# Kernel tuning notes

Measured on AMD Instinct MI355X. Metric: run time of the kernel, lower is better.

Reference implementation:

```python
import jax, jax.numpy as jnp
import numpy as np

N_NODES = 100000
N_EDGES = 1600000
IN_F = 64
HIDDEN = [64, 64, 32]


def _glorot(key, shape):
    limit = float(np.sqrt(6.0 / (shape[0] + shape[1])))
    return jax.random.uniform(key, shape, jnp.float32, -limit, limit)


def setup_inputs() -> dict:
    key = jax.random.key(0)
    ks = jax.random.split(key, 5)
    x = jax.random.normal(ks[0], (N_NODES, IN_F), jnp.float32)
    edge_index = jax.random.randint(ks[1], (2, N_EDGES), 0, N_NODES, jnp.int64)
    dims = [IN_F] + HIDDEN
    params = {}
    for i in range(len(HIDDEN)):
        params[f"W{i+1}"] = _glorot(ks[2 + i], (dims[i], dims[i + 1]))
        params[f"b{i+1}"] = jnp.zeros((dims[i + 1],), jnp.float32)
    return {"x": x, "edge_index": edge_index, **params}


def _gcn_layer(x, src, dst, norm, W, b, n):
    # PyG GCNConv: linear transform, then normalized scatter-sum aggregation, then bias
    h = x @ W                                  # [N, out]
    msg = norm[:, None] * h[src]               # gather + edge scaling, [E+N, out]
    out = jax.ops.segment_sum(msg, dst, num_segments=n)
    return out + b


def reference(x, edge_index, W1, b1, W2, b2, W3, b3):
    n = x.shape[0]
    # add self-loops (GCNConv default add_self_loops=True)
    loops = jnp.arange(n, dtype=edge_index.dtype)
    src = jnp.concatenate([edge_index[0], loops])
    dst = jnp.concatenate([edge_index[1], loops])
    # symmetric normalization: deg over destination (col), norm = d^-1/2[src]*d^-1/2[dst]
    deg = jax.ops.segment_sum(jnp.ones_like(src, x.dtype), dst, num_segments=n)
    dinv = jnp.where(deg > 0, jax.lax.rsqrt(deg), 0.0)
    norm = dinv[src] * dinv[dst]
    h = jax.nn.relu(_gcn_layer(x, src, dst, norm, W1, b1, n))
    h = jax.nn.relu(_gcn_layer(h, src, dst, norm, W2, b2, n))
    return _gcn_layer(h, src, dst, norm, W3, b3, n)
```

## Files before the change

### kernel.cpp

```cpp
#include <hip/hip_runtime.h>
#include <hip/hip_bf16.h>


#define BLOCK 256
#define NBUCKET 512
#define CHUNK 4096
#define SLOT 4608
#define MAX_NPB 256

typedef float f32x4 __attribute__((ext_vector_type(4)));

__device__ __forceinline__ float4 fma4(float s, float4 a, float4 b) {
  return make_float4(fmaf(s, a.x, b.x), fmaf(s, a.y, b.y),
                     fmaf(s, a.z, b.z), fmaf(s, a.w, b.w));
}

__device__ __forceinline__ unsigned int bf16r(float f) {
  unsigned int u = __float_as_uint(f);
  u += 0x7fffu + ((u >> 16) & 1u);
  return u >> 16;
}

__device__ __forceinline__ void acc_bf8(float4& lo, float4& hi, uint4 u) {
  lo.x += __uint_as_float(u.x << 16);
  lo.y += __uint_as_float(u.x & 0xffff0000u);
  lo.z += __uint_as_float(u.y << 16);
  lo.w += __uint_as_float(u.y & 0xffff0000u);
  hi.x += __uint_as_float(u.z << 16);
  hi.y += __uint_as_float(u.z & 0xffff0000u);
  hi.z += __uint_as_float(u.w << 16);
  hi.w += __uint_as_float(u.w & 0xffff0000u);
}


__global__ __launch_bounds__(BLOCK) void binning_kernel(
    const int* __restrict__ src, const int* __restrict__ dst,
    int* __restrict__ bcursor, int* __restrict__ binned, int e, int npb) {
  __shared__ int h[NBUCKET];
  __shared__ int base[NBUCKET];
  for (int i = threadIdx.x; i < NBUCKET; i += BLOCK) h[i] = 0;
  __syncthreads();
  const int cbase = blockIdx.x * CHUNK;
#pragma unroll
  for (int k = 0; k < CHUNK; k += BLOCK * 4) {
    int i = cbase + k + threadIdx.x * 4;
    if (i + 3 < e) {
      int4 d4 = *(const int4*)(dst + i);
      atomicAdd(&h[d4.x / npb], 1);
      atomicAdd(&h[d4.y / npb], 1);
      atomicAdd(&h[d4.z / npb], 1);
      atomicAdd(&h[d4.w / npb], 1);
    } else {
      for (int t = 0; t < 4; ++t)
        if (i + t < e) atomicAdd(&h[dst[i + t] / npb], 1);
    }
  }
  __syncthreads();
  for (int i = threadIdx.x; i < NBUCKET; i += BLOCK) {
    int c = h[i];
    base[i] = c ? atomicAdd(&bcursor[i], c) : 0;
    h[i] = 0;
  }
  __syncthreads();
#pragma unroll
  for (int k = 0; k < CHUNK; k += BLOCK * 4) {
    int i = cbase + k + threadIdx.x * 4;
    if (i + 3 < e) {
      int4 d4 = *(const int4*)(dst + i);
      int4 s4 = *(const int4*)(src + i);
      int b0 = d4.x / npb, b1 = d4.y / npb, b2 = d4.z / npb, b3 = d4.w / npb;
      int o0 = atomicAdd(&h[b0], 1);
      int o1 = atomicAdd(&h[b1], 1);
      int o2 = atomicAdd(&h[b2], 1);
      int o3 = atomicAdd(&h[b3], 1);
      binned[b0 * SLOT + base[b0] + o0] = s4.x | ((d4.x - b0 * npb) << 17);
      binned[b1 * SLOT + base[b1] + o1] = s4.y | ((d4.y - b1 * npb) << 17);
      binned[b2 * SLOT + base[b2] + o2] = s4.z | ((d4.z - b2 * npb) << 17);
      binned[b3 * SLOT + base[b3] + o3] = s4.w | ((d4.w - b3 * npb) << 17);
    } else {
      for (int t = 0; t < 4; ++t) {
        if (i + t < e) {
          int d = dst[i + t];
          int bkt = d / npb;
          int lofs = atomicAdd(&h[bkt], 1);
          binned[bkt * SLOT + base[bkt] + lofs] =
              src[i + t] | ((d - bkt * npb) << 17);
        }
      }
    }
  }
}

__global__ __launch_bounds__(BLOCK) void bucket_build(
    const int* __restrict__ binned, const int* __restrict__ bcursor,
    int* __restrict__ offs, int* __restrict__ cnt, float* __restrict__ dinv,
    int* __restrict__ csr_src, int n, int npb) {
  __shared__ int nhist[MAX_NPB];
  __shared__ int noff[MAX_NPB];
  __shared__ int lcsr[SLOT];
  const int b = blockIdx.x;
  const int node_base = b * npb;
  const int nodes = min(npb, n - node_base);
  if (nodes <= 0) return;
  const int ebase = b * SLOT;
  const int ecnt = bcursor[b];
  for (int i = threadIdx.x; i < npb; i += BLOCK) nhist[i] = 0;
  __syncthreads();
  for (int i = threadIdx.x; i < ecnt; i += BLOCK)
    atomicAdd(&nhist[binned[ebase + i] >> 17], 1);
  __syncthreads();
  if (threadIdx.x < 64) {
    const int lane = threadIdx.x;
    const int bi = lane * 4;
    int v0 = (bi + 0 < nodes) ? nhist[bi + 0] : 0;
    int v1 = (bi + 1 < nodes) ? nhist[bi + 1] : 0;
    int v2 = (bi + 2 < nodes) ? nhist[bi + 2] : 0;
    int v3 = (bi + 3 < nodes) ? nhist[bi + 3] : 0;
    int tsum = v0 + v1 + v2 + v3;
    int s = tsum;
#pragma unroll
    for (int o = 1; o < 64; o <<= 1) {
      int u = __shfl_up(s, o, 64);
      if (lane >= o) s += u;
    }
    int texcl = s - tsum;
    if (bi + 0 < nodes) noff[bi + 0] = texcl;
    if (bi + 1 < nodes) noff[bi + 1] = texcl + v0;
    if (bi + 2 < nodes) noff[bi + 2] = texcl + v0 + v1;
    if (bi + 3 < nodes) noff[bi + 3] = texcl + v0 + v1 + v2;
  }
  __syncthreads();
  for (int i = threadIdx.x; i < nodes; i += BLOCK) {
    int c = nhist[i];
    offs[node_base + i] = ebase + noff[i];
    cnt[node_base + i] = c;
    dinv[node_base + i] = rsqrtf((float)(c + 1));
  }
  __syncthreads();
  for (int i = threadIdx.x; i < ecnt; i += BLOCK) {
    int v = binned[ebase + i];
    int pos = atomicAdd(&noff[v >> 17], 1);
    lcsr[pos] = v & 0x1ffff;
  }
  __syncthreads();
  for (int i = threadIdx.x; i < ecnt; i += BLOCK)
    csr_src[ebase + i] = lcsr[i];
}


__global__ __launch_bounds__(BLOCK) void gemm1_kernel(
    const float* __restrict__ x, const float* __restrict__ W,
    const float* __restrict__ dinv, unsigned short* __restrict__ hbf, int n) {
  __shared__ float Ws[64 * 64];
  for (int i = threadIdx.x * 4; i < 64 * 64; i += BLOCK * 4)
    *(float4*)(Ws + i) = *(const float4*)(W + i);
  __syncthreads();
  const int row = blockIdx.x * 16 + (int)(threadIdx.x >> 4);
  const int c4 = (threadIdx.x & 15) * 4;
  if (row >= n) return;
  const float* xr = x + (size_t)row * 64;
  float4 acc = make_float4(0.f, 0.f, 0.f, 0.f);
#pragma unroll
  for (int k = 0; k < 64; k += 4) {
    f32x4 xn = __builtin_nontemporal_load((const f32x4*)(xr + k));
    float4 w0 = *(const float4*)(Ws + (k + 0) * 64 + c4);
    float4 w1 = *(const float4*)(Ws + (k + 1) * 64 + c4);
    float4 w2 = *(const float4*)(Ws + (k + 2) * 64 + c4);
    float4 w3 = *(const float4*)(Ws + (k + 3) * 64 + c4);
    acc = fma4(xn.x, w0, acc);
    acc = fma4(xn.y, w1, acc);
    acc = fma4(xn.z, w2, acc);
    acc = fma4(xn.w, w3, acc);
  }
  float d = dinv[row];
  uint2 packed;
  packed.x = bf16r(d * acc.x) | (bf16r(d * acc.y) << 16);
  packed.y = bf16r(d * acc.z) | (bf16r(d * acc.w) << 16);
  *(uint2*)(hbf + (size_t)row * 64 + c4) = packed;
}

__global__ __launch_bounds__(BLOCK) void fused_agg_gemm64(
    const unsigned short* __restrict__ hin, const int* __restrict__ csr_src,
    const int* __restrict__ offs, const int* __restrict__ cnt,
    const float* __restrict__ dinv, const float* __restrict__ bias,
    const float* __restrict__ Wn, unsigned short* __restrict__ hout, int n) {
  __shared__ float Ws[64 * 64];
  __shared__ float vrow[16][68];
  for (int i = threadIdx.x * 4; i < 64 * 64; i += BLOCK * 4)
    *(float4*)(Ws + i) = *(const float4*)(Wn + i);
  __syncthreads();
  const int g = threadIdx.x >> 4;
  const int lane16 = threadIdx.x & 15;
  const int colgrp = lane16 & 7;
  const int half = lane16 >> 3;
  const int c8 = colgrp * 8;
  const int node = blockIdx.x * 16 + g;
  const bool valid = node < n;
  float dnode = 0.f;
  if (valid) {
    const int start = offs[node];
    const int cn = cnt[node];
    const unsigned short* hcol = hin + c8;
    float4 l0 = make_float4(0.f, 0.f, 0.f, 0.f), h0 = l0;
    float4 l1 = l0, h1 = l0, l2 = l0, h2 = l0, l3 = l0, h3 = l0;
    if (half == 0)
      acc_bf8(l0, h0, *(const uint4*)(hcol + (size_t)node * 64));
    int j = half * 4;
    for (; j + 4 <= cn; j += 8) {
      int s0 = csr_src[start + j + 0];
      int s1 = csr_src[start + j + 1];
      int s2 = csr_src[start + j + 2];
      int s3 = csr_src[start + j + 3];
      uint4 u0 = *(const uint4*)(hcol + (size_t)s0 * 64);
      uint4 u1 = *(const uint4*)(hcol + (size_t)s1 * 64);
      uint4 u2 = *(const uint4*)(hcol + (size_t)s2 * 64);
      uint4 u3 = *(const uint4*)(hcol + (size_t)s3 * 64);
      acc_bf8(l0, h0, u0);
      acc_bf8(l1, h1, u1);
      acc_bf8(l2, h2, u2);
      acc_bf8(l3, h3, u3);
    }
    if (j < cn) {
      int rem = cn - j;
      int s0 = csr_src[start + j];
      acc_bf8(l1, h1, *(const uint4*)(hcol + (size_t)s0 * 64));
      if (rem > 1) {
        int s1 = csr_src[start + j + 1];
        acc_bf8(l2, h2, *(const uint4*)(hcol + (size_t)s1 * 64));
      }
      if (rem > 2) {
        int s2 = csr_src[start + j + 2];
        acc_bf8(l3, h3, *(const uint4*)(hcol + (size_t)s2 * 64));
      }
    }
    float4 alo = make_float4((l0.x + l1.x) + (l2.x + l3.x),
                             (l0.y + l1.y) + (l2.y + l3.y),
                             (l0.z + l1.z) + (l2.z + l3.z),
                             (l0.w + l1.w) + (l2.w + l3.w));
    float4 ahi = make_float4((h0.x + h1.x) + (h2.x + h3.x),
                             (h0.y + h1.y) + (h2.y + h3.y),
                             (h0.z + h1.z) + (h2.z + h3.z),
                             (h0.w + h1.w) + (h2.w + h3.w));
    alo.x += __shfl_xor(alo.x, 8); alo.y += __shfl_xor(alo.y, 8);
    alo.z += __shfl_xor(alo.z, 8); alo.w += __shfl_xor(alo.w, 8);
    ahi.x += __shfl_xor(ahi.x, 8); ahi.y += __shfl_xor(ahi.y, 8);
    ahi.z += __shfl_xor(ahi.z, 8); ahi.w += __shfl_xor(ahi.w, 8);
    dnode = dinv[node];
    if (half == 0) {
      float4 blo = *(const float4*)(bias + c8);
      float4 bhi = *(const float4*)(bias + c8 + 4);
      float4 vlo = make_float4(fmaxf(fmaf(dnode, alo.x, blo.x), 0.f),
                               fmaxf(fmaf(dnode, alo.y, blo.y), 0.f),
                               fmaxf(fmaf(dnode, alo.z, blo.z), 0.f),
                               fmaxf(fmaf(dnode, alo.w, blo.w), 0.f));
      float4 vhi = make_float4(fmaxf(fmaf(dnode, ahi.x, bhi.x), 0.f),
                               fmaxf(fmaf(dnode, ahi.y, bhi.y), 0.f),
                               fmaxf(fmaf(dnode, ahi.z, bhi.z), 0.f),
                               fmaxf(fmaf(dnode, ahi.w, bhi.w), 0.f));
      *(float4*)(&vrow[g][c8]) = vlo;
      *(float4*)(&vrow[g][c8 + 4]) = vhi;
    }
  }
  if (valid) {
    const int cc = lane16 * 4;
    float4 a0 = make_float4(0.f, 0.f, 0.f, 0.f);
#pragma unroll
    for (int k = 0; k < 64; k += 4) {
      float4 rv = *(const float4*)(&vrow[g][k]);
      a0 = fma4(rv.x, *(const float4*)(Ws + (k + 0) * 64 + cc), a0);
      a0 = fma4(rv.y, *(const float4*)(Ws + (k + 1) * 64 + cc), a0);
      a0 = fma4(rv.z, *(const float4*)(Ws + (k + 2) * 64 + cc), a0);
      a0 = fma4(rv.w, *(const float4*)(Ws + (k + 3) * 64 + cc), a0);
    }
    uint2 packed;
    packed.x = bf16r(dnode * a0.x) | (bf16r(dnode * a0.y) << 16);
    packed.y = bf16r(dnode * a0.z) | (bf16r(dnode * a0.w) << 16);
    *(uint2*)(hout + (size_t)node * 64 + cc) = packed;
  }
}

__global__ __launch_bounds__(BLOCK) void fused_agg_gemm32(
    const unsigned short* __restrict__ hin, const int* __restrict__ csr_src,
    const int* __restrict__ offs, const int* __restrict__ cnt,
    const float* __restrict__ dinv, const float* __restrict__ bias,
    const float* __restrict__ Wn, unsigned short* __restrict__ hout, int n) {
  __shared__ float Ws[64 * 32];
  __shared__ float vrow[32][68];
  for (int i = threadIdx.x * 4; i < 64 * 32; i += BLOCK * 4)
    *(float4*)(Ws + i) = *(const float4*)(Wn + i);
  __syncthreads();
  const int g = threadIdx.x >> 3;
  const int lane8 = threadIdx.x & 7;
  const int c8 = lane8 * 8;
  const int node = blockIdx.x * 32 + g;
  const bool valid = node < n;
  float dnode = 0.f;
  if (valid) {
    const int start = offs[node];
    const int cn = cnt[node];
    const unsigned short* hcol = hin + c8;
    float4 l0 = make_float4(0.f, 0.f, 0.f, 0.f), h0 = l0;
    float4 l1 = l0, h1 = l0, l2 = l0, h2 = l0, l3 = l0, h3 = l0;
    acc_bf8(l0, h0, *(const uint4*)(hcol + (size_t)node * 64));
    int j = 0;
    for (; j + 4 <= cn; j += 4) {
      int s0 = csr_src[start + j + 0];
      int s1 = csr_src[start + j + 1];
      int s2 = csr_src[start + j + 2];
      int s3 = csr_src[start + j + 3];
      uint4 u0 = *(const uint4*)(hcol + (size_t)s0 * 64);
      uint4 u1 = *(const uint4*)(hcol + (size_t)s1 * 64);
      uint4 u2 = *(const uint4*)(hcol + (size_t)s2 * 64);
      uint4 u3 = *(const uint4*)(hcol + (size_t)s3 * 64);
      acc_bf8(l0, h0, u0);
      acc_bf8(l1, h1, u1);
      acc_bf8(l2, h2, u2);
      acc_bf8(l3, h3, u3);
    }
    if (j + 2 <= cn) {
      int s0 = csr_src[start + j + 0];
      int s1 = csr_src[start + j + 1];
      uint4 u0 = *(const uint4*)(hcol + (size_t)s0 * 64);
      uint4 u1 = *(const uint4*)(hcol + (size_t)s1 * 64);
      acc_bf8(l1, h1, u0);
      acc_bf8(l2, h2, u1);
      j += 2;
    }
    if (j < cn) {
      int s0 = csr_src[start + j];
      acc_bf8(l3, h3, *(const uint4*)(hcol + (size_t)s0 * 64));
    }
    float4 alo = make_float4((l0.x + l1.x) + (l2.x + l3.x),
                             (l0.y + l1.y) + (l2.y + l3.y),
                             (l0.z + l1.z) + (l2.z + l3.z),
                             (l0.w + l1.w) + (l2.w + l3.w));
    float4 ahi = make_float4((h0.x + h1.x) + (h2.x + h3.x),
                             (h0.y + h1.y) + (h2.y + h3.y),
                             (h0.z + h1.z) + (h2.z + h3.z),
                             (h0.w + h1.w) + (h2.w + h3.w));
    dnode = dinv[node];
    float4 blo = *(const float4*)(bias + c8);
    float4 bhi = *(const float4*)(bias + c8 + 4);
    float4 vlo = make_float4(fmaxf(fmaf(dnode, alo.x, blo.x), 0.f),
                             fmaxf(fmaf(dnode, alo.y, blo.y), 0.f),
                             fmaxf(fmaf(dnode, alo.z, blo.z), 0.f),
                             fmaxf(fmaf(dnode, alo.w, blo.w), 0.f));
    float4 vhi = make_float4(fmaxf(fmaf(dnode, ahi.x, bhi.x), 0.f),
                             fmaxf(fmaf(dnode, ahi.y, bhi.y), 0.f),
                             fmaxf(fmaf(dnode, ahi.z, bhi.z), 0.f),
                             fmaxf(fmaf(dnode, ahi.w, bhi.w), 0.f));
    *(float4*)(&vrow[g][c8]) = vlo;
    *(float4*)(&vrow[g][c8 + 4]) = vhi;
  }
  if (valid) {
    const int cc = lane8 * 4;
    float4 a0 = make_float4(0.f, 0.f, 0.f, 0.f);
#pragma unroll
    for (int k = 0; k < 64; k += 4) {
      float4 rv = *(const float4*)(&vrow[g][k]);
      a0 = fma4(rv.x, *(const float4*)(Ws + (k + 0) * 32 + cc), a0);
      a0 = fma4(rv.y, *(const float4*)(Ws + (k + 1) * 32 + cc), a0);
      a0 = fma4(rv.z, *(const float4*)(Ws + (k + 2) * 32 + cc), a0);
      a0 = fma4(rv.w, *(const float4*)(Ws + (k + 3) * 32 + cc), a0);
    }
    uint2 packed;
    packed.x = bf16r(dnode * a0.x) | (bf16r(dnode * a0.y) << 16);
    packed.y = bf16r(dnode * a0.z) | (bf16r(dnode * a0.w) << 16);
    *(uint2*)(hout + (size_t)node * 32 + cc) = packed;
  }
}

__global__ __launch_bounds__(BLOCK) void agg3_kernel(
    const unsigned short* __restrict__ hbf, const int* __restrict__ csr_src,
    const int* __restrict__ offs, const int* __restrict__ cnt,
    const float* __restrict__ dinv, const float* __restrict__ bias,
    float* __restrict__ out, int n) {
  constexpr int F = 32;
  const int node = blockIdx.x * 64 + (int)(threadIdx.x >> 2);
  const int c8 = (threadIdx.x & 3) * 8;
  if (node >= n) return;
  const int start = offs[node];
  const int cn = cnt[node];
  const unsigned short* hcol = hbf + c8;
  float4 l0 = make_float4(0.f, 0.f, 0.f, 0.f), h0 = l0;
  float4 l1 = l0, h1 = l0, l2 = l0, h2 = l0, l3 = l0, h3 = l0;
  acc_bf8(l0, h0, *(const uint4*)(hcol + (size_t)node * F));
  int j = 0;
  for (; j + 4 <= cn; j += 4) {
    int s0 = csr_src[start + j + 0];
    int s1 = csr_src[start + j + 1];
    int s2 = csr_src[start + j + 2];
    int s3 = csr_src[start + j + 3];
    uint4 u0 = *(const uint4*)(hcol + (size_t)s0 * F);
    uint4 u1 = *(const uint4*)(hcol + (size_t)s1 * F);
    uint4 u2 = *(const uint4*)(hcol + (size_t)s2 * F);
    uint4 u3 = *(const uint4*)(hcol + (size_t)s3 * F);
    acc_bf8(l0, h0, u0);
    acc_bf8(l1, h1, u1);
    acc_bf8(l2, h2, u2);
    acc_bf8(l3, h3, u3);
  }
  if (j + 2 <= cn) {
    int s0 = csr_src[start + j + 0];
    int s1 = csr_src[start + j + 1];
    uint4 u0 = *(const uint4*)(hcol + (size_t)s0 * F);
    uint4 u1 = *(const uint4*)(hcol + (size_t)s1 * F);
    acc_bf8(l1, h1, u0);
    acc_bf8(l2, h2, u1);
    j += 2;
  }
  if (j < cn) {
    int s0 = csr_src[start + j];
    acc_bf8(l3, h3, *(const uint4*)(hcol + (size_t)s0 * F));
  }
  float4 alo = make_float4((l0.x + l1.x) + (l2.x + l3.x),
                           (l0.y + l1.y) + (l2.y + l3.y),
                           (l0.z + l1.z) + (l2.z + l3.z),
                           (l0.w + l1.w) + (l2.w + l3.w));
  float4 ahi = make_float4((h0.x + h1.x) + (h2.x + h3.x),
                           (h0.y + h1.y) + (h2.y + h3.y),
                           (h0.z + h1.z) + (h2.z + h3.z),
                           (h0.w + h1.w) + (h2.w + h3.w));
  float d = dinv[node];
  float4 blo = *(const float4*)(bias + c8);
  float4 bhi = *(const float4*)(bias + c8 + 4);
  f32x4 vlo = {fmaf(d, alo.x, blo.x), fmaf(d, alo.y, blo.y),
               fmaf(d, alo.z, blo.z), fmaf(d, alo.w, blo.w)};
  f32x4 vhi = {fmaf(d, ahi.x, bhi.x), fmaf(d, ahi.y, bhi.y),
               fmaf(d, ahi.z, bhi.z), fmaf(d, ahi.w, bhi.w)};
  float* op = out + (size_t)node * F + c8;
  __builtin_nontemporal_store(vlo, (f32x4*)op);
  __builtin_nontemporal_store(vhi, (f32x4*)(op + 4));
}

static inline size_t align_up(size_t v, size_t a) { return (v + a - 1) & ~(a - 1); }

extern "C" void kernel_launch(void* const* d_in, const int* in_sizes, int n_in,
                              void* d_out, int out_size, void* d_ws, size_t ws_size,
                              hipStream_t stream) {
  const float* x = (const float*)d_in[0];
  const int* edge_index = (const int*)d_in[1];
  const float* W1 = (const float*)d_in[2];
  const float* b1 = (const float*)d_in[3];
  const float* W2 = (const float*)d_in[4];
  const float* b2 = (const float*)d_in[5];
  const float* W3 = (const float*)d_in[6];
  const float* b3 = (const float*)d_in[7];
  float* out = (float*)d_out;

  const int n = in_sizes[0] / 64;
  const int e = in_sizes[1] / 2;
  const int* e_src = edge_index;
  const int* e_dst = edge_index + e;
  const int npb = (n + NBUCKET - 1) / NBUCKET;

  char* ws = (char*)d_ws;
  size_t off = 0;
  int* bcursor = (int*)(ws + off); off = align_up(off + NBUCKET * 4, 512);
  int* offs    = (int*)(ws + off); off = align_up(off + (size_t)n * 4, 512);
  int* cnt     = (int*)(ws + off); off = align_up(off + (size_t)n * 4, 512);
  float* dinv  = (float*)(ws + off); off = align_up(off + (size_t)n * 4, 512);
  int* binned  = (int*)(ws + off); off = align_up(off + (size_t)NBUCKET * SLOT * 4, 512);
  int* csr_src = (int*)(ws + off); off = align_up(off + (size_t)NBUCKET * SLOT * 4, 512);
  unsigned short* hbuf_a = (unsigned short*)(ws + off);
  off = align_up(off + (size_t)n * 64 * 2, 512);
  unsigned short* hbuf_b = (unsigned short*)(ws + off);
  off = align_up(off + (size_t)n * 64 * 2, 512);
  (void)ws_size;

  const int gC = (e + CHUNK - 1) / CHUNK;

  hipMemsetAsync(bcursor, 0, NBUCKET * 4, stream);
  binning_kernel<<<gC, BLOCK, 0, stream>>>(e_src, e_dst, bcursor, binned, e, npb);
  bucket_build<<<NBUCKET, BLOCK, 0, stream>>>(binned, bcursor, offs, cnt, dinv,
                                              csr_src, n, npb);

  gemm1_kernel<<<(n + 15) / 16, BLOCK, 0, stream>>>(x, W1, dinv, hbuf_a, n);
  fused_agg_gemm64<<<(n + 15) / 16, BLOCK, 0, stream>>>(
      hbuf_a, csr_src, offs, cnt, dinv, b1, W2, hbuf_b, n);
  fused_agg_gemm32<<<(n + 31) / 32, BLOCK, 0, stream>>>(
      hbuf_b, csr_src, offs, cnt, dinv, b2, W3, hbuf_a, n);
  agg3_kernel<<<(n + 63) / 64, BLOCK, 0, stream>>>(hbuf_a, csr_src, offs, cnt,
                                                   dinv, b3, out, n);
}
```

Before: 249.0 us.

## Use split-bf16 MFMA for dense transforms in all three GCN layers

Replaces the scalar FP32 FMA GEMMs in gemm1 and the two fused aggregate+GEMM kernels with MFMA 16x16x32 bf16 instructions. Both operands are split into hi/lo bf16 parts, and three MFMAs per K-chunk keep accuracy close to FP32. A small prep kernel pre-transposes and splits the weights once per call, which removes the per-block FP32 weight staging in LDS. The cost is extra split arithmetic, an added launch, and output stores that become scattered 2-byte writes instead of packed 8-byte ones.

```diff
diff --git a/kernel.cpp b/kernel.cpp
--- a/kernel.cpp
+++ b/kernel.cpp
@@ -9,6 +9,7 @@
 #define MAX_NPB 256
 
 typedef float f32x4 __attribute__((ext_vector_type(4)));
+typedef short bf16x8 __attribute__((ext_vector_type(8)));
 
 __device__ __forceinline__ float4 fma4(float s, float4 a, float4 b) {
   return make_float4(fmaf(s, a.x, b.x), fmaf(s, a.y, b.y),
@@ -19,6 +20,13 @@
   unsigned int u = __float_as_uint(f);
   u += 0x7fffu + ((u >> 16) & 1u);
   return u >> 16;
+}
+
+__device__ __forceinline__ void bsplit(float v, unsigned int& h,
+                                       unsigned int& l) {
+  h = bf16r(v);
+  float r = v - __uint_as_float(h << 16);
+  l = bf16r(r);
 }
 
 __device__ __forceinline__ void acc_bf8(float4& lo, float4& hi, uint4 u) {
@@ -147,48 +155,101 @@
     csr_src[ebase + i] = lcsr[i];
 }
 
+__global__ __launch_bounds__(BLOCK) void wprep_kernel(
+    const float* __restrict__ W1, const float* __restrict__ W2,
+    const float* __restrict__ W3, unsigned short* __restrict__ Wt) {
+  int t = blockIdx.x * BLOCK + threadIdx.x;
+  float v;
+  int hi_off, lo_off;
+  if (t < 4096) {
+    int nn = t >> 6, k = t & 63;
+    v = W1[k * 64 + nn];
+    hi_off = t;
+    lo_off = 4096 + t;
+  } else if (t < 8192) {
+    int i = t - 4096;
+    int nn = i >> 6, k = i & 63;
+    v = W2[k * 64 + nn];
+    hi_off = 8192 + i;
+    lo_off = 12288 + i;
+  } else {
+    int i = t - 8192;
+    if (i >= 2048) return;
+    int nn = i >> 6, k = i & 63;
+    v = W3[k * 32 + nn];
+    hi_off = 16384 + i;
+    lo_off = 18432 + i;
+  }
+  unsigned int h, l;
+  bsplit(v, h, l);
+  Wt[hi_off] = (unsigned short)h;
+  Wt[lo_off] = (unsigned short)l;
+}
+
 
 __global__ __launch_bounds__(BLOCK) void gemm1_kernel(
-    const float* __restrict__ x, const float* __restrict__ W,
+    const float* __restrict__ x, const unsigned short* __restrict__ Wt,
     const float* __restrict__ dinv, unsigned short* __restrict__ hbf, int n) {
-  __shared__ float Ws[64 * 64];
-  for (int i = threadIdx.x * 4; i < 64 * 64; i += BLOCK * 4)
-    *(float4*)(Ws + i) = *(const float4*)(W + i);
-  __syncthreads();
-  const int row = blockIdx.x * 16 + (int)(threadIdx.x >> 4);
+  __shared__ unsigned short Ahi[16][72];
+  __shared__ unsigned short Alo[16][72];
+  __shared__ float dvs[16];
+  const int r16 = threadIdx.x >> 4;
   const int c4 = (threadIdx.x & 15) * 4;
-  if (row >= n) return;
-  const float* xr = x + (size_t)row * 64;
-  float4 acc = make_float4(0.f, 0.f, 0.f, 0.f);
+  const int node = blockIdx.x * 16 + r16;
+  const int wv = threadIdx.x >> 6;
+  const int fr = threadIdx.x & 15;
+  const int fq = (threadIdx.x >> 4) & 3;
+  const unsigned short* wb = Wt + ((wv * 16 + fr) * 64) + fq * 8;
+  bf16x8 bh0 = *(const bf16x8*)(wb);
+  bf16x8 bh1 = *(const bf16x8*)(wb + 32);
+  bf16x8 bl0 = *(const bf16x8*)(wb + 4096);
+  bf16x8 bl1 = *(const bf16x8*)(wb + 4096 + 32);
+  uint2 ph = make_uint2(0u, 0u), pl = make_uint2(0u, 0u);
+  if (node < n) {
+    f32x4 xv =
+        __builtin_nontemporal_load((const f32x4*)(x + (size_t)node * 64 + c4));
+    unsigned int h0, l0, h1, l1, h2, l2, h3, l3;
+    bsplit(xv.x, h0, l0);
+    bsplit(xv.y, h1, l1);
+    bsplit(xv.z, h2, l2);
+    bsplit(xv.w, h3, l3);
+    ph = make_uint2(h0 | (h1 << 16), h2 | (h3 << 16));
+    pl = make_uint2(l0 | (l1 << 16), l2 | (l3 << 16));
+  }
+  *(uint2*)(&Ahi[r16][c4]) = ph;
+  *(uint2*)(&Alo[r16][c4]) = pl;
+  if ((threadIdx.x & 15) == 0) dvs[r16] = (node < n) ? dinv[node] : 0.f;
+  __syncthreads();
+  bf16x8 ah0 = *(const bf16x8*)(&Ahi[fr][fq * 8]);
+  bf16x8 ah1 = *(const bf16x8*)(&Ahi[fr][fq * 8 + 32]);
+  bf16x8 aL0 = *(const bf16x8*)(&Alo[fr][fq * 8]);
+  bf16x8 aL1 = *(const bf16x8*)(&Alo[fr][fq * 8 + 32]);
+  f32x4 acc = {0.f, 0.f, 0.f, 0.f};
+  acc = __builtin_amdgcn_mfma_f32_16x16x32_bf16(ah0, bh0, acc, 0, 0, 0);
+  acc = __builtin_amdgcn_mfma_f32_16x16x32_bf16(aL0, bh0, acc, 0, 0, 0);
+  acc = __builtin_amdgcn_mfma_f32_16x16x32_bf16(ah0, bl0, acc, 0, 0, 0);
+  acc = __builtin_amdgcn_mfma_f32_16x16x32_bf16(ah1, bh1, acc, 0, 0, 0);
+  acc = __builtin_amdgcn_mfma_f32_16x16x32_bf16(aL1, bh1, acc, 0, 0, 0);
+  acc = __builtin_amdgcn_mfma_f32_16x16x32_bf16(ah1, bl1, acc, 0, 0, 0);
+  const int col = wv * 16 + fr;
 #pragma unroll
-  for (int k = 0; k < 64; k += 4) {
-    f32x4 xn = __builtin_nontemporal_load((const f32x4*)(xr + k));
-    float4 w0 = *(const float4*)(Ws + (k + 0) * 64 + c4);
-    float4 w1 = *(const float4*)(Ws + (k + 1) * 64 + c4);
-    float4 w2 = *(const float4*)(Ws + (k + 2) * 64 + c4);
-    float4 w3 = *(const float4*)(Ws + (k + 3) * 64 + c4);
-    acc = fma4(xn.x, w0, acc);
-    acc = fma4(xn.y, w1, acc);
-    acc = fma4(xn.z, w2, acc);
-    acc = fma4(xn.w, w3, acc);
-  }
-  float d = dinv[row];
-  uint2 packed;
-  packed.x = bf16r(d * acc.x) | (bf16r(d * acc.y) << 16);
-  packed.y = bf16r(d * acc.z) | (bf16r(d * acc.w) << 16);
-  *(uint2*)(hbf + (size_t)row * 64 + c4) = packed;
+  for (int j = 0; j < 4; ++j) {
+    int row = fq * 4 + j;
+    int nd = blockIdx.x * 16 + row;
+    if (nd < n)
+      hbf[(size_t)nd * 64 + col] = (unsigned short)bf16r(dvs[row] * acc[j]);
+  }
 }
 
 __global__ __launch_bounds__(BLOCK) void fused_agg_gemm64(
     const unsigned short* __restrict__ hin, const int* __restrict__ csr_src,
     const int* __restrict__ offs, const int* __restrict__ cnt,
     const float* __restrict__ dinv, const float* __restrict__ bias,
-    const float* __restrict__ Wn, unsigned short* __restrict__ hout, int n) {
-  __shared__ float Ws[64 * 64];
-  __shared__ float vrow[16][68];
-  for (int i = threadIdx.x * 4; i < 64 * 64; i += BLOCK * 4)
-    *(float4*)(Ws + i) = *(const float4*)(Wn + i);
-  __syncthreads();
+    const unsigned short* __restrict__ Wt, unsigned short* __restrict__ hout,
+    int n) {
+  __shared__ unsigned short Ahi[16][72];
+  __shared__ unsigned short Alo[16][72];
+  __shared__ float dvs[16];
   const int g = threadIdx.x >> 4;
   const int lane16 = threadIdx.x & 15;
   const int colgrp = lane16 & 7;
@@ -197,6 +258,7 @@
   const int node = blockIdx.x * 16 + g;
   const bool valid = node < n;
   float dnode = 0.f;
+  uint4 qh = make_uint4(0u, 0u, 0u, 0u), ql = make_uint4(0u, 0u, 0u, 0u);
   if (valid) {
     const int start = offs[node];
     const int cn = cnt[node];
@@ -247,35 +309,60 @@
     ahi.z += __shfl_xor(ahi.z, 8); ahi.w += __shfl_xor(ahi.w, 8);
     dnode = dinv[node];
     if (half == 0) {
-      float4 blo = *(const float4*)(bias + c8);
-      float4 bhi = *(const float4*)(bias + c8 + 4);
-      float4 vlo = make_float4(fmaxf(fmaf(dnode, alo.x, blo.x), 0.f),
-                               fmaxf(fmaf(dnode, alo.y, blo.y), 0.f),
-                               fmaxf(fmaf(dnode, alo.z, blo.z), 0.f),
-                               fmaxf(fmaf(dnode, alo.w, blo.w), 0.f));
-      float4 vhi = make_float4(fmaxf(fmaf(dnode, ahi.x, bhi.x), 0.f),
-                               fmaxf(fmaf(dnode, ahi.y, bhi.y), 0.f),
-                               fmaxf(fmaf(dnode, ahi.z, bhi.z), 0.f),
-                               fmaxf(fmaf(dnode, ahi.w, bhi.w), 0.f));
-      *(float4*)(&vrow[g][c8]) = vlo;
-      *(float4*)(&vrow[g][c8 + 4]) = vhi;
-    }
-  }
-  if (valid) {
-    const int cc = lane16 * 4;
-    float4 a0 = make_float4(0.f, 0.f, 0.f, 0.f);
+      float4 b4l = *(const float4*)(bias + c8);
+      float4 b4h = *(const float4*)(bias + c8 + 4);
+      float v0 = fmaxf(fmaf(dnode, alo.x, b4l.x), 0.f);
+      float v1 = fmaxf(fmaf(dnode, alo.y, b4l.y), 0.f);
+      float v2 = fmaxf(fmaf(dnode, alo.z, b4l.z), 0.f);
+      float v3 = fmaxf(fmaf(dnode, alo.w, b4l.w), 0.f);
+      float v4 = fmaxf(fmaf(dnode, ahi.x, b4h.x), 0.f);
+      float v5 = fmaxf(fmaf(dnode, ahi.y, b4h.y), 0.f);
+      float v6 = fmaxf(fmaf(dnode, ahi.z, b4h.z), 0.f);
+      float v7 = fmaxf(fmaf(dnode, ahi.w, b4h.w), 0.f);
+      unsigned int h0u, l0u, h1u, l1u, h2u, l2u, h3u, l3u;
+      unsigned int h4u, l4u, h5u, l5u, h6u, l6u, h7u, l7u;
+      bsplit(v0, h0u, l0u); bsplit(v1, h1u, l1u);
+      bsplit(v2, h2u, l2u); bsplit(v3, h3u, l3u);
+      bsplit(v4, h4u, l4u); bsplit(v5, h5u, l5u);
+      bsplit(v6, h6u, l6u); bsplit(v7, h7u, l7u);
+      qh = make_uint4(h0u | (h1u << 16), h2u | (h3u << 16),
+                      h4u | (h5u << 16), h6u | (h7u << 16));
+      ql = make_uint4(l0u | (l1u << 16), l2u | (l3u << 16),
+                      l4u | (l5u << 16), l6u | (l7u << 16));
+    }
+  }
+  if (half == 0) {
+    *(uint4*)(&Ahi[g][c8]) = qh;
+    *(uint4*)(&Alo[g][c8]) = ql;
+    if (lane16 == 0) dvs[g] = dnode;
+  }
+  const int wv = threadIdx.x >> 6;
+  const int fr = threadIdx.x & 15;
+  const int fq = (threadIdx.x >> 4) & 3;
+  const unsigned short* wb = Wt + ((wv * 16 + fr) * 64) + fq * 8;
+  bf16x8 bh0 = *(const bf16x8*)(wb);
+  bf16x8 bh1 = *(const bf16x8*)(wb + 32);
+  bf16x8 bl0 = *(const bf16x8*)(wb + 4096);
+  bf16x8 bl1 = *(const bf16x8*)(wb + 4096 + 32);
+  __syncthreads();
+  bf16x8 ah0 = *(const bf16x8*)(&Ahi[fr][fq * 8]);
+  bf16x8 ah1 = *(const bf16x8*)(&Ahi[fr][fq * 8 + 32]);
+  bf16x8 aL0 = *(const bf16x8*)(&Alo[fr][fq * 8]);
+  bf16x8 aL1 = *(const bf16x8*)(&Alo[fr][fq * 8 + 32]);
+  f32x4 acc = {0.f, 0.f, 0.f, 0.f};
+  acc = __builtin_amdgcn_mfma_f32_16x16x32_bf16(ah0, bh0, acc, 0, 0, 0);
+  acc = __builtin_amdgcn_mfma_f32_16x16x32_bf16(aL0, bh0, acc, 0, 0, 0);
+  acc = __builtin_amdgcn_mfma_f32_16x16x32_bf16(ah0, bl0, acc, 0, 0, 0);
+  acc = __builtin_amdgcn_mfma_f32_16x16x32_bf16(ah1, bh1, acc, 0, 0, 0);
+  acc = __builtin_amdgcn_mfma_f32_16x16x32_bf16(aL1, bh1, acc, 0, 0, 0);
+  acc = __builtin_amdgcn_mfma_f32_16x16x32_bf16(ah1, bl1, acc, 0, 0, 0);
+  const int col = wv * 16 + fr;
 #pragma unroll
-    for (int k = 0; k < 64; k += 4) {
-      float4 rv = *(const float4*)(&vrow[g][k]);
-      a0 = fma4(rv.x, *(const float4*)(Ws + (k + 0) * 64 + cc), a0);
-      a0 = fma4(rv.y, *(const float4*)(Ws + (k + 1) * 64 + cc), a0);
-      a0 = fma4(rv.z, *(const float4*)(Ws + (k + 2) * 64 + cc), a0);
-      a0 = fma4(rv.w, *(const float4*)(Ws + (k + 3) * 64 + cc), a0);
-    }
-    uint2 packed;
-    packed.x = bf16r(dnode * a0.x) | (bf16r(dnode * a0.y) << 16);
-    packed.y = bf16r(dnode * a0.z) | (bf16r(dnode * a0.w) << 16);
-    *(uint2*)(hout + (size_t)node * 64 + cc) = packed;
+  for (int j = 0; j < 4; ++j) {
+    int row = fq * 4 + j;
+    int nd = blockIdx.x * 16 + row;
+    if (nd < n)
+      hout[(size_t)nd * 64 + col] = (unsigned short)bf16r(dvs[row] * acc[j]);
   }
 }
 
@@ -283,18 +370,18 @@
     const unsigned short* __restrict__ hin, const int* __restrict__ csr_src,
     const int* __restrict__ offs, const int* __restrict__ cnt,
     const float* __restrict__ dinv, const float* __restrict__ bias,
-    const float* __restrict__ Wn, unsigned short* __restrict__ hout, int n) {
-  __shared__ float Ws[64 * 32];
-  __shared__ float vrow[32][68];
-  for (int i = threadIdx.x * 4; i < 64 * 32; i += BLOCK * 4)
-    *(float4*)(Ws + i) = *(const float4*)(Wn + i);
-  __syncthreads();
+    const unsigned short* __restrict__ Wt, unsigned short* __restrict__ hout,
+    int n) {
+  __shared__ unsigned short Ahi[32][72];
+  __shared__ unsigned short Alo[32][72];
+  __shared__ float dvs[32];
   const int g = threadIdx.x >> 3;
   const int lane8 = threadIdx.x & 7;
   const int c8 = lane8 * 8;
   const int node = blockIdx.x * 32 + g;
   const bool valid = node < n;
   float dnode = 0.f;
+  uint4 qh = make_uint4(0u, 0u, 0u, 0u), ql = make_uint4(0u, 0u, 0u, 0u);
   if (valid) {
     const int start = offs[node];
     const int cn = cnt[node];
@@ -339,34 +426,59 @@
                              (h0.z + h1.z) + (h2.z + h3.z),
                              (h0.w + h1.w) + (h2.w + h3.w));
     dnode = dinv[node];
-    float4 blo = *(const float4*)(bias + c8);
-    float4 bhi = *(const float4*)(bias + c8 + 4);
-    float4 vlo = make_float4(fmaxf(fmaf(dnode, alo.x, blo.x), 0.f),
-                             fmaxf(fmaf(dnode, alo.y, blo.y), 0.f),
-                             fmaxf(fmaf(dnode, alo.z, blo.z), 0.f),
-                             fmaxf(fmaf(dnode, alo.w, blo.w), 0.f));
-    float4 vhi = make_float4(fmaxf(fmaf(dnode, ahi.x, bhi.x), 0.f),
-                             fmaxf(fmaf(dnode, ahi.y, bhi.y), 0.f),
-                             fmaxf(fmaf(dnode, ahi.z, bhi.z), 0.f),
-                             fmaxf(fmaf(dnode, ahi.w, bhi.w), 0.f));
-    *(float4*)(&vrow[g][c8]) = vlo;
-    *(float4*)(&vrow[g][c8 + 4]) = vhi;
-  }
-  if (valid) {
-    const int cc = lane8 * 4;
-    float4 a0 = make_float4(0.f, 0.f, 0.f, 0.f);
+    float4 b4l = *(const float4*)(bias + c8);
+    float4 b4h = *(const float4*)(bias + c8 + 4);
+    float v0 = fmaxf(fmaf(dnode, alo.x, b4l.x), 0.f);
+    float v1 = fmaxf(fmaf(dnode, alo.y, b4l.y), 0.f);
+    float v2 = fmaxf(fmaf(dnode, alo.z, b4l.z), 0.f);
+    float v3 = fmaxf(fmaf(dnode, alo.w, b4l.w), 0.f);
+    float v4 = fmaxf(fmaf(dnode, ahi.x, b4h.x), 0.f);
+    float v5 = fmaxf(fmaf(dnode, ahi.y, b4h.y), 0.f);
+    float v6 = fmaxf(fmaf(dnode, ahi.z, b4h.z), 0.f);
+    float v7 = fmaxf(fmaf(dnode, ahi.w, b4h.w), 0.f);
+    unsigned int h0u, l0u, h1u, l1u, h2u, l2u, h3u, l3u;
+    unsigned int h4u, l4u, h5u, l5u, h6u, l6u, h7u, l7u;
+    bsplit(v0, h0u, l0u); bsplit(v1, h1u, l1u);
+    bsplit(v2, h2u, l2u); bsplit(v3, h3u, l3u);
+    bsplit(v4, h4u, l4u); bsplit(v5, h5u, l5u);
+    bsplit(v6, h6u, l6u); bsplit(v7, h7u, l7u);
+    qh = make_uint4(h0u | (h1u << 16), h2u | (h3u << 16),
+                    h4u | (h5u << 16), h6u | (h7u << 16));
+    ql = make_uint4(l0u | (l1u << 16), l2u | (l3u << 16),
+                    l4u | (l5u << 16), l6u | (l7u << 16));
+  }
+  *(uint4*)(&Ahi[g][c8]) = qh;
+  *(uint4*)(&Alo[g][c8]) = ql;
+  if (lane8 == 0) dvs[g] = dnode;
+  const int wv = threadIdx.x >> 6;
+  const int mt = wv >> 1;
+  const int nt = wv & 1;
+  const int fr = threadIdx.x & 15;
+  const int fq = (threadIdx.x >> 4) & 3;
+  const unsigned short* wb = Wt + ((nt * 16 + fr) * 64) + fq * 8;
+  bf16x8 bh0 = *(const bf16x8*)(wb);
+  bf16x8 bh1 = *(const bf16x8*)(wb + 32);
+  bf16x8 bl0 = *(const bf16x8*)(wb + 2048);
+  bf16x8 bl1 = *(const bf16x8*)(wb + 2048 + 32);
+  __syncthreads();
+  bf16x8 ah0 = *(const bf16x8*)(&Ahi[mt * 16 + fr][fq * 8]);
+  bf16x8 ah1 = *(const bf16x8*)(&Ahi[mt * 16 + fr][fq * 8 + 32]);
+  bf16x8 aL0 = *(const bf16x8*)(&Alo[mt * 16 + fr][fq * 8]);
+  bf16x8 aL1 = *(const bf16x8*)(&Alo[mt * 16 + fr][fq * 8 + 32]);
+  f32x4 acc = {0.f, 0.f, 0.f, 0.f};
+  acc = __builtin_amdgcn_mfma_f32_16x16x32_bf16(ah0, bh0, acc, 0, 0, 0);
+  acc = __builtin_amdgcn_mfma_f32_16x16x32_bf16(aL0, bh0, acc, 0, 0, 0);
+  acc = __builtin_amdgcn_mfma_f32_16x16x32_bf16(ah0, bl0, acc, 0, 0, 0);
+  acc = __builtin_amdgcn_mfma_f32_16x16x32_bf16(ah1, bh1, acc, 0, 0, 0);
+  acc = __builtin_amdgcn_mfma_f32_16x16x32_bf16(aL1, bh1, acc, 0, 0, 0);
+  acc = __builtin_amdgcn_mfma_f32_16x16x32_bf16(ah1, bl1, acc, 0, 0, 0);
+  const int col = nt * 16 + fr;
 #pragma unroll
-    for (int k = 0; k < 64; k += 4) {
-      float4 rv = *(const float4*)(&vrow[g][k]);
-      a0 = fma4(rv.x, *(const float4*)(Ws + (k + 0) * 32 + cc), a0);
-      a0 = fma4(rv.y, *(const float4*)(Ws + (k + 1) * 32 + cc), a0);
-      a0 = fma4(rv.z, *(const float4*)(Ws + (k + 2) * 32 + cc), a0);
-      a0 = fma4(rv.w, *(const float4*)(Ws + (k + 3) * 32 + cc), a0);
-    }
-    uint2 packed;
-    packed.x = bf16r(dnode * a0.x) | (bf16r(dnode * a0.y) << 16);
-    packed.y = bf16r(dnode * a0.z) | (bf16r(dnode * a0.w) << 16);
-    *(uint2*)(hout + (size_t)node * 32 + cc) = packed;
+  for (int j = 0; j < 4; ++j) {
+    int row = mt * 16 + fq * 4 + j;
+    int nd = blockIdx.x * 32 + row;
+    if (nd < n)
+      hout[(size_t)nd * 32 + col] = (unsigned short)bf16r(dvs[row] * acc[j]);
   }
 }
 
@@ -466,20 +578,27 @@
   off = align_up(off + (size_t)n * 64 * 2, 512);
   unsigned short* hbuf_b = (unsigned short*)(ws + off);
   off = align_up(off + (size_t)n * 64 * 2, 512);
+  unsigned short* Wt = (unsigned short*)(ws + off);
+  off = align_up(off + (size_t)20480 * 2, 512);
   (void)ws_size;
 
+  unsigned short* Wt1 = Wt;
+  unsigned short* Wt2 = Wt + 8192;
+  unsigned short* Wt3 = Wt + 16384;
+
   const int gC = (e + CHUNK - 1) / CHUNK;
 
   hipMemsetAsync(bcursor, 0, NBUCKET * 4, stream);
+  wprep_kernel<<<40, BLOCK, 0, stream>>>(W1, W2, W3, Wt);
   binning_kernel<<<gC, BLOCK, 0, stream>>>(e_src, e_dst, bcursor, binned, e, npb);
   bucket_build<<<NBUCKET, BLOCK, 0, stream>>>(binned, bcursor, offs, cnt, dinv,
                                               csr_src, n, npb);
 
-  gemm1_kernel<<<(n + 15) / 16, BLOCK, 0, stream>>>(x, W1, dinv, hbuf_a, n);
+  gemm1_kernel<<<(n + 15) / 16, BLOCK, 0, stream>>>(x, Wt1, dinv, hbuf_a, n);
   fused_agg_gemm64<<<(n + 15) / 16, BLOCK, 0, stream>>>(
-      hbuf_a, csr_src, offs, cnt, dinv, b1, W2, hbuf_b, n);
+      hbuf_a, csr_src, offs, cnt, dinv, b1, Wt2, hbuf_b, n);
   fused_agg_gemm32<<<(n + 31) / 32, BLOCK, 0, stream>>>(
-      hbuf_b, csr_src, offs, cnt, dinv, b2, W3, hbuf_a, n);
+      hbuf_b, csr_src, offs, cnt, dinv, b2, Wt3, hbuf_a, n);
   agg3_kernel<<<(n + 63) / 64, BLOCK, 0, stream>>>(hbuf_a, csr_src, offs, cnt,
                                                    dinv, b3, out, n);
 }
```

Measured after the change: 242.8 us. 1.03x faster.
